# Optimization experiments

Measured on AMD Instinct MI355X. Metric: run time of the kernel, lower is better.

## Reference

```python
import jax, jax.numpy as jnp
import numpy as np

B = 131072
D = 64
H1 = 512
H2 = 256
NC = 128  # nurse classes
DC = 128  # doctor classes
EPS = 1e-5
NEG = -1e9


def _kaiming(key, fan_in, fan_out):
    # kaiming_normal_ with mode='fan_out', relu gain: std = sqrt(2/fan_out)
    return jax.random.normal(key, (fan_in, fan_out), jnp.float32) * jnp.sqrt(2.0 / fan_out)


def setup_inputs() -> dict:
    key = jax.random.key(0)
    ks = jax.random.split(key, 16)
    x = jax.random.normal(ks[0], (B, D), jnp.float32)
    sn = jax.random.randint(ks[1], (B,), 0, NC)
    sd = jax.random.randint(ks[2], (B,), 0, DC)
    # last-4 / last-3 columns carry the per-sample max class thresholds
    x = x.at[:, -4].set(sn.astype(jnp.float32)).at[:, -3].set(sd.astype(jnp.float32))
    inp = {
        'x': x,
        'W0': _kaiming(ks[3], D, H1), 'b0': jnp.zeros((H1,), jnp.float32),
        'g0': jnp.ones((H1,), jnp.float32), 'be0': jnp.zeros((H1,), jnp.float32),
        'rm0': jax.random.normal(ks[4], (H1,), jnp.float32) * 0.1,
        'rv0': jax.random.uniform(ks[5], (H1,), jnp.float32, 0.5, 1.5),
        'W1': _kaiming(ks[6], H1, H2), 'b1': jnp.zeros((H2,), jnp.float32),
        'g1': jnp.ones((H2,), jnp.float32), 'be1': jnp.zeros((H2,), jnp.float32),
        'rm1': jax.random.normal(ks[7], (H2,), jnp.float32) * 0.1,
        'rv1': jax.random.uniform(ks[8], (H2,), jnp.float32, 0.5, 1.5),
        'nW1': _kaiming(ks[9], H2, 64), 'nb1': jnp.zeros((64,), jnp.float32),
        'nW2': _kaiming(ks[10], 64, NC), 'nb2': jnp.zeros((NC,), jnp.float32),
        'dW1': _kaiming(ks[11], H2, 64), 'db1': jnp.zeros((64,), jnp.float32),
        'dW2': _kaiming(ks[12], 64, DC), 'db2': jnp.zeros((DC,), jnp.float32),
    }
    return inp


def _bn(h, g, be, rm, rv):
    # BatchNorm1d inference: normalize with running stats
    return (h - rm) * (g * jax.lax.rsqrt(rv + EPS)) + be


def reference(x, W0, b0, g0, be0, rm0, rv0, W1, b1, g1, be1, rm1, rv1,
              nW1, nb1, nW2, nb2, dW1, db1, dW2, db2):
    s_nurse = x[:, -4].astype(jnp.int32)   # [B]
    s_doctor = x[:, -3].astype(jnp.int32)  # [B]

    h = jax.nn.relu(_bn(x @ W0 + b0, g0, be0, rm0, rv0))   # [B,H1]
    h = jax.nn.relu(_bn(h @ W1 + b1, g1, be1, rm1, rv1))   # [B,H2]

    nurse_logits = jax.nn.relu(h @ nW1 + nb1) @ nW2 + nb2   # [B,NC]
    doctor_logits = jax.nn.relu(h @ dW1 + db1) @ dW2 + db2  # [B,DC]

    # vectorized range mask: positions <= s_max are kept
    nmask = (jnp.arange(NC)[None, :] <= s_nurse[:, None]).astype(nurse_logits.dtype)
    dmask = (jnp.arange(DC)[None, :] <= s_doctor[:, None]).astype(doctor_logits.dtype)
    nurse_logits = nurse_logits * nmask + (1.0 - nmask) * NEG
    doctor_logits = doctor_logits * dmask + (1.0 - dmask) * NEG
    return (nurse_logits, doctor_logits)
```

## Files before the change

kernel.cpp:

```cpp
#include <hip/hip_runtime.h>

#define NB 131072
#define NEG9 -1e9f

typedef __attribute__((ext_vector_type(8))) __bf16 bf16x8;
typedef __attribute__((ext_vector_type(4))) float f32x4;
typedef __attribute__((ext_vector_type(2))) unsigned int u32x2;
typedef __attribute__((ext_vector_type(4))) unsigned int u32x4;

__device__ __forceinline__ f32x4 mfma16(bf16x8 a, bf16x8 b, f32x4 c) {
    return __builtin_amdgcn_mfma_f32_16x16x32_bf16(a, b, c, 0, 0, 0);
}

__device__ __forceinline__ unsigned pk(float h, float l) {
    return __builtin_amdgcn_perm(__builtin_bit_cast(unsigned, h),
                                 __builtin_bit_cast(unsigned, l), 0x07060302u);
}
__device__ __forceinline__ unsigned pku(unsigned h, unsigned l) {
    return __builtin_amdgcn_perm(h, l, 0x07060302u);
}

__device__ __forceinline__ unsigned short f2bf(float f) {
    unsigned u = __builtin_bit_cast(unsigned, f);
    u += 0x7fffu + ((u >> 16) & 1u);
    return (unsigned short)(u >> 16);
}

struct __align__(16) Wspace {
    unsigned short W0t[512][64];
    unsigned short W1t[256][512];
    unsigned short nW1t[64][256];
    unsigned short dW1t[64][256];
    unsigned short nW2t[128][64];
    unsigned short dW2t[128][64];
    float c0[512];
    float c1[256];
    float nb1c[64], db1c[64];
    float nb2c[128], db2c[128];
};

__device__ Wspace g_ws;

__global__ __launch_bounds__(256) void prep_kernel(
    const float* __restrict__ W0, const float* __restrict__ b0,
    const float* __restrict__ g0, const float* __restrict__ be0,
    const float* __restrict__ rm0, const float* __restrict__ rv0,
    const float* __restrict__ W1, const float* __restrict__ b1,
    const float* __restrict__ g1, const float* __restrict__ be1,
    const float* __restrict__ rm1, const float* __restrict__ rv1,
    const float* __restrict__ nW1, const float* __restrict__ nb1,
    const float* __restrict__ nW2, const float* __restrict__ nb2,
    const float* __restrict__ dW1, const float* __restrict__ db1,
    const float* __restrict__ dW2, const float* __restrict__ db2)
{
    const int b = blockIdx.x;
    const int t = threadIdx.x;

    if (b == 52) {
        {
            int i = t;          g_ws.c0[i] = (b0[i] - rm0[i]) * (g0[i] * rsqrtf(rv0[i] + 1e-5f)) + be0[i];
            i = t + 256;        g_ws.c0[i] = (b0[i] - rm0[i]) * (g0[i] * rsqrtf(rv0[i] + 1e-5f)) + be0[i];
        }
        g_ws.c1[t] = (b1[t] - rm1[t]) * (g1[t] * rsqrtf(rv1[t] + 1e-5f)) + be1[t];
        if (t < 64)  { g_ws.nb1c[t] = nb1[t]; g_ws.db1c[t] = db1[t]; }
        if (t < 128) { g_ws.nb2c[t] = nb2[t]; g_ws.db2c[t] = db2[t]; }
        return;
    }

    const float* src; unsigned short* dst;
    const float* gp = nullptr; const float* rvp = nullptr;
    int sld, dld, k0, n0;
    if (b < 32)      { src = W1;  dst = (unsigned short*)g_ws.W1t;  sld = 256; dld = 512;
                       k0 = (b >> 2) * 64; n0 = (b & 3) * 64; gp = g1; rvp = rv1; }
    else if (b < 40) { src = W0;  dst = (unsigned short*)g_ws.W0t;  sld = 512; dld = 64;
                       k0 = 0; n0 = (b - 32) * 64; gp = g0; rvp = rv0; }
    else if (b < 44) { src = nW1; dst = (unsigned short*)g_ws.nW1t; sld = 64;  dld = 256;
                       k0 = (b - 40) * 64; n0 = 0; }
    else if (b < 48) { src = dW1; dst = (unsigned short*)g_ws.dW1t; sld = 64;  dld = 256;
                       k0 = (b - 44) * 64; n0 = 0; }
    else if (b < 50) { src = nW2; dst = (unsigned short*)g_ws.nW2t; sld = 128; dld = 64;
                       k0 = 0; n0 = (b - 48) * 64; }
    else             { src = dW2; dst = (unsigned short*)g_ws.dW2t; sld = 128; dld = 64;
                       k0 = 0; n0 = (b - 50) * 64; }

    __shared__ unsigned short tile[64][66];

    const int rr = t >> 4;
    const int cc = (t & 15) * 4;

#pragma unroll
    for (int g = 0; g < 4; ++g) {
        const int r = rr + g * 16;
        f32x4 v = *(const f32x4*)&src[(size_t)(k0 + r) * sld + n0 + cc];
        if (gp) {
            f32x4 gv = *(const f32x4*)&gp[n0 + cc];
            f32x4 rv = *(const f32x4*)&rvp[n0 + cc];
            v[0] *= gv[0] * rsqrtf(rv[0] + 1e-5f);
            v[1] *= gv[1] * rsqrtf(rv[1] + 1e-5f);
            v[2] *= gv[2] * rsqrtf(rv[2] + 1e-5f);
            v[3] *= gv[3] * rsqrtf(rv[3] + 1e-5f);
        }
        *(unsigned*)&tile[r][cc]     = (unsigned)f2bf(v[0]) | ((unsigned)f2bf(v[1]) << 16);
        *(unsigned*)&tile[r][cc + 2] = (unsigned)f2bf(v[2]) | ((unsigned)f2bf(v[3]) << 16);
    }
    __syncthreads();

#pragma unroll
    for (int g = 0; g < 4; ++g) {
        const int n = rr + g * 16;
        unsigned o01 = (unsigned)tile[cc + 0][n] | ((unsigned)tile[cc + 1][n] << 16);
        unsigned o23 = (unsigned)tile[cc + 2][n] | ((unsigned)tile[cc + 3][n] << 16);
        u32x2 o = { o01, o23 };
        *(u32x2*)&dst[(size_t)(n0 + n) * dld + k0 + cc] = o;
    }
}

__global__ __launch_bounds__(512, 4) void fused_mlp(
    const u32x4* __restrict__ xu, float* __restrict__ out)
{
    __shared__ __align__(16) unsigned short sXs[8 * 128 * 8];
    __shared__ __align__(16) unsigned short sH[32 * 128 * 8];

    const int tid = threadIdx.x;
    const int w = tid >> 6;
    const int lane = tid & 63;
    const int m = lane & 15;
    const int q = lane >> 4;
    const int qh = q >> 1;
    const int ql = (q & 1) * 4;
    const int row0 = blockIdx.x * 128;

    {
        int r = tid >> 3, g = tid & 7;
#pragma unroll
        for (int hh = 0; hh < 2; ++hh) {
            int rr = r + hh * 64;
            u32x4 v0 = __builtin_nontemporal_load(&xu[(size_t)(row0 + rr) * 16 + g * 2]);
            u32x4 v1 = __builtin_nontemporal_load(&xu[(size_t)(row0 + rr) * 16 + g * 2 + 1]);
            u32x4 p = { pku(v0[1], v0[0]), pku(v0[3], v0[2]), pku(v1[1], v1[0]), pku(v1[3], v1[2]) };
            *(u32x4*)&sXs[(g * 128 + rr) * 8] = p;
        }
    }
    __syncthreads();

    f32x4 acc1[2][8];
#pragma unroll
    for (int a = 0; a < 2; ++a)
#pragma unroll
        for (int b = 0; b < 8; ++b) acc1[a][b] = f32x4{0.f, 0.f, 0.f, 0.f};

    for (int ch = 0; ch < 2; ++ch) {
#pragma unroll
        for (int nt = 0; nt < 2; ++nt) {
            const int gcb = ch * 256 + w * 32 + nt * 16;
            bf16x8 wa0 = *(const bf16x8*)&g_ws.W0t[gcb + m][q * 8];
            bf16x8 wa1 = *(const bf16x8*)&g_ws.W0t[gcb + m][32 + q * 8];
            f32x4 bias = *(const f32x4*)&g_ws.c0[gcb + q * 4];
            const int kg = w * 4 + nt * 2 + qh;
#pragma unroll
            for (int mt = 0; mt < 8; ++mt) {
                bf16x8 xq0 = *(const bf16x8*)&sXs[(q * 128 + mt * 16 + m) * 8];
                bf16x8 xq1 = *(const bf16x8*)&sXs[((4 + q) * 128 + mt * 16 + m) * 8];
                f32x4 c = {0.f, 0.f, 0.f, 0.f};
                c = mfma16(wa0, xq0, c);
                c = mfma16(wa1, xq1, c);
                u32x2 pw = { pk(fmaxf(c[1] + bias[1], 0.f), fmaxf(c[0] + bias[0], 0.f)),
                             pk(fmaxf(c[3] + bias[3], 0.f), fmaxf(c[2] + bias[2], 0.f)) };
                *(u32x2*)&sH[(kg * 128 + mt * 16 + m) * 8 + ql] = pw;
            }
        }
        __syncthreads();

#pragma unroll
        for (int ks = 0; ks < 8; ++ks) {
            bf16x8 wb0 = *(const bf16x8*)&g_ws.W1t[w * 32 + m][ch * 256 + ks * 32 + q * 8];
            bf16x8 wb1 = *(const bf16x8*)&g_ws.W1t[w * 32 + 16 + m][ch * 256 + ks * 32 + q * 8];
#pragma unroll
            for (int mt = 0; mt < 8; ++mt) {
                bf16x8 ab = *(const bf16x8*)&sH[((ks * 4 + q) * 128 + mt * 16 + m) * 8];
                acc1[0][mt] = mfma16(wb0, ab, acc1[0][mt]);
                acc1[1][mt] = mfma16(wb1, ab, acc1[1][mt]);
            }
        }
        __syncthreads();
    }

#pragma unroll
    for (int nt = 0; nt < 2; ++nt) {
        const int cb = w * 32 + nt * 16;
        f32x4 bias = *(const f32x4*)&g_ws.c1[cb + q * 4];
        const int kg = w * 4 + nt * 2 + qh;
#pragma unroll
        for (int mt = 0; mt < 8; ++mt) {
            f32x4 c = acc1[nt][mt];
            u32x2 pw = { pk(fmaxf(c[1] + bias[1], 0.f), fmaxf(c[0] + bias[0], 0.f)),
                         pk(fmaxf(c[3] + bias[3], 0.f), fmaxf(c[2] + bias[2], 0.f)) };
            *(u32x2*)&sH[(kg * 128 + mt * 16 + m) * 8 + ql] = pw;
        }
    }
    __syncthreads();

    const int head = w >> 2;
    {
        const int cb = (w & 3) * 16;
        const unsigned short (*Wh)[256] = head ? g_ws.dW1t : g_ws.nW1t;
        const float* bh = head ? g_ws.db1c : g_ws.nb1c;
        f32x4 acc[8];
#pragma unroll
        for (int b = 0; b < 8; ++b) acc[b] = f32x4{0.f, 0.f, 0.f, 0.f};
#pragma unroll
        for (int ks = 0; ks < 8; ++ks) {
            bf16x8 wh = *(const bf16x8*)&Wh[cb + m][ks * 32 + q * 8];
#pragma unroll
            for (int mt = 0; mt < 8; ++mt) {
                bf16x8 ab = *(const bf16x8*)&sH[((ks * 4 + q) * 128 + mt * 16 + m) * 8];
                acc[mt] = mfma16(wh, ab, acc[mt]);
            }
        }
        __syncthreads();
        unsigned short* Ah = sH + head * 8192;
        f32x4 bias = *(const f32x4*)&bh[cb + q * 4];
        const int kg = (w & 3) * 2 + qh;
#pragma unroll
        for (int mt = 0; mt < 8; ++mt) {
            f32x4 c = acc[mt];
            u32x2 pw = { pk(fmaxf(c[1] + bias[1], 0.f), fmaxf(c[0] + bias[0], 0.f)),
                         pk(fmaxf(c[3] + bias[3], 0.f), fmaxf(c[2] + bias[2], 0.f)) };
            *(u32x2*)&Ah[(kg * 128 + mt * 16 + m) * 8 + ql] = pw;
        }
    }
    __syncthreads();

    {
        const unsigned short (*W2)[64] = head ? g_ws.dW2t : g_ws.nW2t;
        const float* b2 = head ? g_ws.db2c : g_ws.nb2c;
        const unsigned short* Ah = sH + head * 8192;
        float* op = out + (size_t)head * (size_t)NB * 128;

        int thr[8];
#pragma unroll
        for (int mt = 0; mt < 8; ++mt) {
            unsigned tv = *(const unsigned*)&sXs[(7 * 128 + mt * 16 + m) * 8 + 4];
            thr[mt] = (int)__builtin_bit_cast(float, head ? (tv & 0xffff0000u) : (tv << 16));
        }
#pragma unroll
        for (int ct = 0; ct < 2; ++ct) {
            const int ocb = (w & 3) * 32 + ct * 16;
            bf16x8 w0 = *(const bf16x8*)&W2[ocb + m][q * 8];
            bf16x8 w1 = *(const bf16x8*)&W2[ocb + m][32 + q * 8];
            f32x4 bias = *(const f32x4*)&b2[ocb + q * 4];
#pragma unroll
            for (int mt = 0; mt < 8; ++mt) {
                bf16x8 a0 = *(const bf16x8*)&Ah[(q * 128 + mt * 16 + m) * 8];
                bf16x8 a1 = *(const bf16x8*)&Ah[((4 + q) * 128 + mt * 16 + m) * 8];
                f32x4 c = {0.f, 0.f, 0.f, 0.f};
                c = mfma16(w0, a0, c);
                c = mfma16(w1, a1, c);
                const int ci = ocb + q * 4;
                const int t = thr[mt];
                f32x4 v;
                v[0] = (ci + 0 <= t) ? c[0] + bias[0] : NEG9;
                v[1] = (ci + 1 <= t) ? c[1] + bias[1] : NEG9;
                v[2] = (ci + 2 <= t) ? c[2] + bias[2] : NEG9;
                v[3] = (ci + 3 <= t) ? c[3] + bias[3] : NEG9;
                *(f32x4*)&op[(size_t)(row0 + mt * 16 + m) * 128 + ci] = v;
            }
        }
    }
}

extern "C" void kernel_launch(void* const* d_in, const int* in_sizes, int n_in,
                              void* d_out, int out_size, void* d_ws, size_t ws_size,
                              hipStream_t stream) {
    (void)in_sizes; (void)n_in; (void)d_ws; (void)ws_size;

    prep_kernel<<<53, 256, 0, stream>>>(
        (const float*)d_in[1], (const float*)d_in[2], (const float*)d_in[3],
        (const float*)d_in[4], (const float*)d_in[5], (const float*)d_in[6],
        (const float*)d_in[7], (const float*)d_in[8], (const float*)d_in[9],
        (const float*)d_in[10], (const float*)d_in[11], (const float*)d_in[12],
        (const float*)d_in[13], (const float*)d_in[14], (const float*)d_in[15],
        (const float*)d_in[16], (const float*)d_in[17], (const float*)d_in[18],
        (const float*)d_in[19], (const float*)d_in[20]);

    fused_mlp<<<NB / 128, 512, 0, stream>>>((const u32x4*)d_in[0], (float*)d_out);
}
```

Baseline: 255.9 us.

## Reshape per-warp tiles into 2D blocks to cut LDS fragment reloads

Changes the work split of every MFMA stage after layer 0. Before, each warp covered a narrow column slice across all 128 rows; now each covers a 2D tile (64 cols x 64 rows in layer 1, 32x64 in the hidden heads, 64x64 in the output heads). Each activation fragment read from LDS now feeds more MFMAs, which lowers shared-memory read traffic per MFMA, and each output row segment written is wider and more contiguous. The cost is extra weight-fragment loads from global memory per warp and more accumulator registers, which may lower occupancy.

```diff
diff --git a/kernel.cpp b/kernel.cpp
--- a/kernel.cpp
+++ b/kernel.cpp
@@ -143,11 +143,13 @@
     }
     __syncthreads();
 
-    f32x4 acc1[2][8];
-#pragma unroll
-    for (int a = 0; a < 2; ++a)
-#pragma unroll
-        for (int b = 0; b < 8; ++b) acc1[a][b] = f32x4{0.f, 0.f, 0.f, 0.f};
+    const int cg = w & 3;
+    const int rh = w >> 2;
+    f32x4 acc1[4][4];
+#pragma unroll
+    for (int a = 0; a < 4; ++a)
+#pragma unroll
+        for (int b = 0; b < 4; ++b) acc1[a][b] = f32x4{0.f, 0.f, 0.f, 0.f};
 
     for (int ch = 0; ch < 2; ++ch) {
 #pragma unroll
@@ -173,97 +175,116 @@
 
 #pragma unroll
         for (int ks = 0; ks < 8; ++ks) {
-            bf16x8 wb0 = *(const bf16x8*)&g_ws.W1t[w * 32 + m][ch * 256 + ks * 32 + q * 8];
-            bf16x8 wb1 = *(const bf16x8*)&g_ws.W1t[w * 32 + 16 + m][ch * 256 + ks * 32 + q * 8];
-#pragma unroll
-            for (int mt = 0; mt < 8; ++mt) {
-                bf16x8 ab = *(const bf16x8*)&sH[((ks * 4 + q) * 128 + mt * 16 + m) * 8];
+            bf16x8 wb0 = *(const bf16x8*)&g_ws.W1t[cg * 64 + m][ch * 256 + ks * 32 + q * 8];
+            bf16x8 wb1 = *(const bf16x8*)&g_ws.W1t[cg * 64 + 16 + m][ch * 256 + ks * 32 + q * 8];
+            bf16x8 wb2 = *(const bf16x8*)&g_ws.W1t[cg * 64 + 32 + m][ch * 256 + ks * 32 + q * 8];
+            bf16x8 wb3 = *(const bf16x8*)&g_ws.W1t[cg * 64 + 48 + m][ch * 256 + ks * 32 + q * 8];
+#pragma unroll
+            for (int mt = 0; mt < 4; ++mt) {
+                bf16x8 ab = *(const bf16x8*)&sH[((ks * 4 + q) * 128 + rh * 64 + mt * 16 + m) * 8];
                 acc1[0][mt] = mfma16(wb0, ab, acc1[0][mt]);
                 acc1[1][mt] = mfma16(wb1, ab, acc1[1][mt]);
+                acc1[2][mt] = mfma16(wb2, ab, acc1[2][mt]);
+                acc1[3][mt] = mfma16(wb3, ab, acc1[3][mt]);
             }
         }
         __syncthreads();
     }
 
 #pragma unroll
-    for (int nt = 0; nt < 2; ++nt) {
-        const int cb = w * 32 + nt * 16;
+    for (int nt = 0; nt < 4; ++nt) {
+        const int cb = cg * 64 + nt * 16;
         f32x4 bias = *(const f32x4*)&g_ws.c1[cb + q * 4];
-        const int kg = w * 4 + nt * 2 + qh;
-#pragma unroll
-        for (int mt = 0; mt < 8; ++mt) {
+        const int kg = cg * 8 + nt * 2 + qh;
+#pragma unroll
+        for (int mt = 0; mt < 4; ++mt) {
             f32x4 c = acc1[nt][mt];
             u32x2 pw = { pk(fmaxf(c[1] + bias[1], 0.f), fmaxf(c[0] + bias[0], 0.f)),
                          pk(fmaxf(c[3] + bias[3], 0.f), fmaxf(c[2] + bias[2], 0.f)) };
-            *(u32x2*)&sH[(kg * 128 + mt * 16 + m) * 8 + ql] = pw;
+            *(u32x2*)&sH[(kg * 128 + rh * 64 + mt * 16 + m) * 8 + ql] = pw;
         }
     }
     __syncthreads();
 
     const int head = w >> 2;
+    const int rh1 = w & 1;
+    const int ct2 = (w >> 1) & 1;
     {
-        const int cb = (w & 3) * 16;
         const unsigned short (*Wh)[256] = head ? g_ws.dW1t : g_ws.nW1t;
         const float* bh = head ? g_ws.db1c : g_ws.nb1c;
-        f32x4 acc[8];
-#pragma unroll
-        for (int b = 0; b < 8; ++b) acc[b] = f32x4{0.f, 0.f, 0.f, 0.f};
+        f32x4 acc[2][4];
+#pragma unroll
+        for (int a = 0; a < 2; ++a)
+#pragma unroll
+            for (int b = 0; b < 4; ++b) acc[a][b] = f32x4{0.f, 0.f, 0.f, 0.f};
 #pragma unroll
         for (int ks = 0; ks < 8; ++ks) {
-            bf16x8 wh = *(const bf16x8*)&Wh[cb + m][ks * 32 + q * 8];
-#pragma unroll
-            for (int mt = 0; mt < 8; ++mt) {
-                bf16x8 ab = *(const bf16x8*)&sH[((ks * 4 + q) * 128 + mt * 16 + m) * 8];
-                acc[mt] = mfma16(wh, ab, acc[mt]);
+            bf16x8 wh0 = *(const bf16x8*)&Wh[ct2 * 32 + m][ks * 32 + q * 8];
+            bf16x8 wh1 = *(const bf16x8*)&Wh[ct2 * 32 + 16 + m][ks * 32 + q * 8];
+#pragma unroll
+            for (int mt = 0; mt < 4; ++mt) {
+                bf16x8 ab = *(const bf16x8*)&sH[((ks * 4 + q) * 128 + rh1 * 64 + mt * 16 + m) * 8];
+                acc[0][mt] = mfma16(wh0, ab, acc[0][mt]);
+                acc[1][mt] = mfma16(wh1, ab, acc[1][mt]);
             }
         }
         __syncthreads();
         unsigned short* Ah = sH + head * 8192;
-        f32x4 bias = *(const f32x4*)&bh[cb + q * 4];
-        const int kg = (w & 3) * 2 + qh;
-#pragma unroll
-        for (int mt = 0; mt < 8; ++mt) {
-            f32x4 c = acc[mt];
-            u32x2 pw = { pk(fmaxf(c[1] + bias[1], 0.f), fmaxf(c[0] + bias[0], 0.f)),
-                         pk(fmaxf(c[3] + bias[3], 0.f), fmaxf(c[2] + bias[2], 0.f)) };
-            *(u32x2*)&Ah[(kg * 128 + mt * 16 + m) * 8 + ql] = pw;
+#pragma unroll
+        for (int nt = 0; nt < 2; ++nt) {
+            f32x4 bias = *(const f32x4*)&bh[ct2 * 32 + nt * 16 + q * 4];
+            const int kg = ct2 * 4 + nt * 2 + qh;
+#pragma unroll
+            for (int mt = 0; mt < 4; ++mt) {
+                f32x4 c = acc[nt][mt];
+                u32x2 pw = { pk(fmaxf(c[1] + bias[1], 0.f), fmaxf(c[0] + bias[0], 0.f)),
+                             pk(fmaxf(c[3] + bias[3], 0.f), fmaxf(c[2] + bias[2], 0.f)) };
+                *(u32x2*)&Ah[(kg * 128 + rh1 * 64 + mt * 16 + m) * 8 + ql] = pw;
+            }
         }
     }
     __syncthreads();
 
     {
+        const int ch2 = (w >> 1) & 1;
         const unsigned short (*W2)[64] = head ? g_ws.dW2t : g_ws.nW2t;
         const float* b2 = head ? g_ws.db2c : g_ws.nb2c;
         const unsigned short* Ah = sH + head * 8192;
         float* op = out + (size_t)head * (size_t)NB * 128;
 
-        int thr[8];
-#pragma unroll
-        for (int mt = 0; mt < 8; ++mt) {
-            unsigned tv = *(const unsigned*)&sXs[(7 * 128 + mt * 16 + m) * 8 + 4];
+        int thr[4];
+#pragma unroll
+        for (int mt = 0; mt < 4; ++mt) {
+            unsigned tv = *(const unsigned*)&sXs[(7 * 128 + rh1 * 64 + mt * 16 + m) * 8 + 4];
             thr[mt] = (int)__builtin_bit_cast(float, head ? (tv & 0xffff0000u) : (tv << 16));
         }
-#pragma unroll
-        for (int ct = 0; ct < 2; ++ct) {
-            const int ocb = (w & 3) * 32 + ct * 16;
-            bf16x8 w0 = *(const bf16x8*)&W2[ocb + m][q * 8];
-            bf16x8 w1 = *(const bf16x8*)&W2[ocb + m][32 + q * 8];
-            f32x4 bias = *(const f32x4*)&b2[ocb + q * 4];
-#pragma unroll
-            for (int mt = 0; mt < 8; ++mt) {
-                bf16x8 a0 = *(const bf16x8*)&Ah[(q * 128 + mt * 16 + m) * 8];
-                bf16x8 a1 = *(const bf16x8*)&Ah[((4 + q) * 128 + mt * 16 + m) * 8];
+        bf16x8 w2f[4][2];
+        f32x4 b2f[4];
+#pragma unroll
+        for (int ct = 0; ct < 4; ++ct) {
+            const int ocb = ch2 * 64 + ct * 16;
+            w2f[ct][0] = *(const bf16x8*)&W2[ocb + m][q * 8];
+            w2f[ct][1] = *(const bf16x8*)&W2[ocb + m][32 + q * 8];
+            b2f[ct] = *(const f32x4*)&b2[ocb + q * 4];
+        }
+#pragma unroll
+        for (int mt = 0; mt < 4; ++mt) {
+            bf16x8 a0 = *(const bf16x8*)&Ah[(q * 128 + rh1 * 64 + mt * 16 + m) * 8];
+            bf16x8 a1 = *(const bf16x8*)&Ah[((4 + q) * 128 + rh1 * 64 + mt * 16 + m) * 8];
+            const int t = thr[mt];
+            const size_t orow = (size_t)(row0 + rh1 * 64 + mt * 16 + m) * 128;
+#pragma unroll
+            for (int ct = 0; ct < 4; ++ct) {
                 f32x4 c = {0.f, 0.f, 0.f, 0.f};
-                c = mfma16(w0, a0, c);
-                c = mfma16(w1, a1, c);
-                const int ci = ocb + q * 4;
-                const int t = thr[mt];
+                c = mfma16(w2f[ct][0], a0, c);
+                c = mfma16(w2f[ct][1], a1, c);
+                const int ci = ch2 * 64 + ct * 16 + q * 4;
                 f32x4 v;
-                v[0] = (ci + 0 <= t) ? c[0] + bias[0] : NEG9;
-                v[1] = (ci + 1 <= t) ? c[1] + bias[1] : NEG9;
-                v[2] = (ci + 2 <= t) ? c[2] + bias[2] : NEG9;
-                v[3] = (ci + 3 <= t) ? c[3] + bias[3] : NEG9;
-                *(f32x4*)&op[(size_t)(row0 + mt * 16 + m) * 128 + ci] = v;
+                v[0] = (ci + 0 <= t) ? c[0] + b2f[ct][0] : NEG9;
+                v[1] = (ci + 1 <= t) ? c[1] + b2f[ct][1] : NEG9;
+                v[2] = (ci + 2 <= t) ? c[2] + b2f[ct][2] : NEG9;
+                v[3] = (ci + 3 <= t) ? c[3] + b2f[ct][3] : NEG9;
+                *(f32x4*)&op[orow + ci] = v;
             }
         }
     }
```

Measured after the change: 299.5 us. 17.0% more time.
